# Optimization experiments

Hardware: AMD Instinct MI355X
Metric: run time of the kernel (lower is better)

Reference implementation:

```python
import jax, jax.numpy as jnp
import numpy as np

EPS = 1e-6


def ln_fwd(x, gamma, beta):
    # layernorm over last dim (biased variance), per TTT ln_fwd
    mu = x.mean(-1, keepdims=True)
    var = x.var(-1, keepdims=True)
    xh = (x - mu) * jax.lax.rsqrt(var + EPS)
    return gamma * xh + beta


def ln_fused_l2_bwd(x, l2_target, gamma, beta):
    # grad of 0.5*||LN(x) - target||^2 w.r.t. x, fused (per TTT ln_fused_l2_bwd)
    D = x.shape[-1]
    mu = x.mean(-1, keepdims=True)
    var = x.var(-1, keepdims=True)
    std = jnp.sqrt(var + EPS)
    xh = (x - mu) / std
    y = gamma * xh + beta
    gxh = (y - l2_target) * gamma
    z = (D * gxh - gxh.sum(-1, keepdims=True) - xh * (gxh * xh).sum(-1, keepdims=True)) / (D * std)
    return z


def setup_inputs() -> dict:
    key = jax.random.key(0)
    ks = jax.random.split(key, 5)
    B, nh, nmb, mbs, hd = 8, 8, 256, 16, 64
    XQ = jax.random.normal(ks[0], (B, nh, nmb, mbs, hd), jnp.float32)
    XK = jax.random.normal(ks[1], (B, nh, nmb, mbs, hd), jnp.float32)
    XV = jax.random.normal(ks[2], (B, nh, nmb, mbs, hd), jnp.float32)
    # eta = small positive per-token learning rates (ttt_base_lr/head_dim scale)
    eta = jax.random.uniform(ks[3], (B, nh, nmb, mbs, mbs), jnp.float32) * (1.0 / hd)
    W1 = jax.random.normal(ks[4], (nh, hd, hd), jnp.float32) * 0.02
    b1 = jnp.zeros((nh, 1, hd), jnp.float32)
    ln_weight = jnp.ones((nh * hd,), jnp.float32)
    ln_bias = jnp.zeros((nh * hd,), jnp.float32)
    return {"XQ": XQ, "XK": XK, "XV": XV, "eta": eta, "W1": W1, "b1": b1,
            "ln_weight": ln_weight, "ln_bias": ln_bias}


def reference(XQ, XK, XV, eta, W1, b1, ln_weight, ln_bias):
    B, nh, nmb, mbs, hd = XQ.shape
    lnw = ln_weight.reshape(nh, 1, hd)
    lnb = ln_bias.reshape(nh, 1, hd)
    W1_0 = jnp.broadcast_to(W1[None], (B, nh, hd, hd))
    b1_0 = jnp.broadcast_to(b1[None], (B, nh, 1, hd))
    tril = jnp.tril(jnp.ones((mbs, mbs), XQ.dtype))

    def step(carry, inp):
        W1s, b1s = carry               # [B,nh,hd,hd], [B,nh,1,hd]
        xq, xk, xv, et = inp           # [B,nh,mbs,hd] x3, [B,nh,mbs,mbs]
        Z1 = xk @ W1s + b1s
        g = ln_fused_l2_bwd(Z1, xv - xk, lnw, lnb)          # grad_l_wrt_Z1
        Attn1 = tril * (xq @ jnp.swapaxes(xk, -1, -2))      # causal QK^T
        b1_bar = b1s - (tril * et) @ g
        Z1_bar = xq @ W1s - (et * Attn1) @ g + b1_bar
        last_eta = et[..., -1, :, None]                     # [B,nh,mbs,1]
        W1_last = W1s - jnp.swapaxes(last_eta * xk, -1, -2) @ g
        b1_last = b1s - jnp.sum(last_eta * g, axis=-2, keepdims=True)
        out = xq + ln_fwd(Z1_bar, lnw, lnb)
        return (W1_last, b1_last), out

    xs = (jnp.moveaxis(XQ, 2, 0), jnp.moveaxis(XK, 2, 0),
          jnp.moveaxis(XV, 2, 0), jnp.moveaxis(eta, 2, 0))
    _, outs = jax.lax.scan(step, (W1_0, b1_0), xs)
    # outs: [nmb,B,nh,mbs,hd] -> [B,nmb,mbs,nh,hd] -> [B,L,width]
    return jnp.transpose(outs, (1, 0, 3, 2, 4)).reshape(B, nmb * mbs, nh * hd)
```

## Files before the change

kernel.cpp:

```cpp
#include <hip/hip_runtime.h>
#include <hip/hip_bf16.h>

typedef __attribute__((ext_vector_type(8))) short short8;
typedef __attribute__((ext_vector_type(4))) short short4_t;
typedef __attribute__((ext_vector_type(4))) float f32x4;

constexpr int MBS = 16, HD = 64, NMB = 256;

#define MFMA32(a, b, c) __builtin_amdgcn_mfma_f32_16x16x32_bf16(a, b, c, 0, 0, 0)
#define TR_READ(dst, addr, IMM) \
    asm volatile("ds_read_b64_tr_b16 %0, %1 offset:" IMM : "=&v"(dst) : "v"(addr) : "memory")

union U4S8 { unsigned u[4]; short8 s; };
union U2S4 { unsigned u[2]; short4_t s; };
union FI { float f; int i; };

__device__ inline unsigned pkbf(float a, float b) {
    union { __hip_bfloat162 h; unsigned u; } c;
    c.h = __float22bfloat162_rn(make_float2(a, b));
    return c.u;
}
__device__ inline short8 cmb(short4_t a, short4_t b) {
    short8 r;
    r[0]=a[0]; r[1]=a[1]; r[2]=a[2]; r[3]=a[3];
    r[4]=b[0]; r[5]=b[1]; r[6]=b[2]; r[7]=b[3];
    return r;
}
__device__ inline float dpp16(float x) {
    FI v; v.f = x; FI t;
    t.i = __builtin_amdgcn_update_dpp(0, v.i, 0xB1, 0xf, 0xf, true);  v.f += t.f;
    t.i = __builtin_amdgcn_update_dpp(0, v.i, 0x4E, 0xf, 0xf, true);  v.f += t.f;
    t.i = __builtin_amdgcn_update_dpp(0, v.i, 0x124, 0xf, 0xf, true); v.f += t.f;
    t.i = __builtin_amdgcn_update_dpp(0, v.i, 0x128, 0xf, 0xf, true); v.f += t.f;
    return v.f;
}
__device__ inline void bar() {
    __builtin_amdgcn_sched_barrier(0);
    asm volatile("s_waitcnt lgkmcnt(0)" ::: "memory");
    __builtin_amdgcn_s_barrier();
    __builtin_amdgcn_sched_barrier(0);
}

__global__ __launch_bounds__(256) void ttt_scan(
    const float* __restrict__ gXQ, const float* __restrict__ gXK,
    const float* __restrict__ gXV, const float* __restrict__ gETA,
    const float* __restrict__ gW1, const float* __restrict__ gB1,
    const float* __restrict__ gLNW, const float* __restrict__ gLNB,
    float* __restrict__ gOUT)
{
    __shared__ __align__(16) short sWt[64 * 72];
    __shared__ __align__(16) short bxk[16 * 72];
    __shared__ __align__(16) short bxq[16 * 72];
    __shared__ __align__(16) short sGt[2048];
    __shared__ __align__(16) short sXKe[2048];
    __shared__ __align__(16) short sE[16 * 40];
    __shared__ __align__(16) float sZ1[16 * 68];
    __shared__ __align__(16) float sZb[16 * 68];
    __shared__ __align__(16) float sAttn[16 * 20];
    __shared__ __align__(16) float sEta[2][256];

    const int t  = threadIdx.x;
    const int s  = t >> 4;
    const int dt = t & 15;
    const int lane = t & 63;
    const int w  = t >> 6;
    const int gq = lane >> 4;
    const int lc = lane & 15;
    const int bh = blockIdx.x, b = bh >> 3, h = bh & 7;

    const float* xqg = gXQ + (size_t)bh * (NMB * MBS * HD);
    const float* xkg = gXK + (size_t)bh * (NMB * MBS * HD);
    const float* xvg = gXV + (size_t)bh * (NMB * MBS * HD);
    const float* etg = gETA + (size_t)bh * (NMB * MBS * MBS);

    for (int i = t; i < 2048; i += 256) { sGt[i] = 0; sXKe[i] = 0; }
    for (int i = t; i < 16 * 40; i += 256) sE[i] = 0;

    f32x4 Wacc[4];
#pragma unroll
    for (int ct = 0; ct < 4; ++ct) {
#pragma unroll
        for (int r = 0; r < 4; ++r)
            Wacc[ct][r] = gW1[h * 4096 + (16 * w + 4 * gq + r) * 64 + 16 * ct + lc];
        U2S4 wp;
        wp.u[0] = pkbf(Wacc[ct][0], Wacc[ct][1]);
        wp.u[1] = pkbf(Wacc[ct][2], Wacc[ct][3]);
        *(short4_t*)&sWt[(16 * ct + lc) * 72 + 16 * w + 4 * gq] = wp.s;
    }
    float b1v = gB1[h * 64 + 16 * w + lc];

    const float4 gam = *(const float4*)&gLNW[h * 64 + dt * 4];
    const float4 bet = *(const float4*)&gLNB[h * 64 + dt * 4];
    const float ga[4] = {gam.x, gam.y, gam.z, gam.w};
    const float ba[4] = {bet.x, bet.y, bet.z, bet.w};
    float c1a[4], gba[4];
    float sc1 = 0.f;
#pragma unroll
    for (int c = 0; c < 4; ++c) {
        c1a[c] = ga[c] * ga[c];
        gba[c] = ga[c] * ba[c];
        sc1 += c1a[c];
    }
    sc1 = dpp16(sc1);

    const int ecol = (gq < 2) ? 8 * gq : 0;

    float4 pq = *(const float4*)&xqg[t * 4];
    float4 pk = *(const float4*)&xkg[t * 4];
    float4 pv = *(const float4*)&xvg[t * 4];
    float4 pe = make_float4(0.f, 0.f, 0.f, 0.f);
    if (t < 64) pe = *(const float4*)&etg[t * 4];

    { U2S4 u_; u_.u[0]=pkbf(pk.x,pk.y); u_.u[1]=pkbf(pk.z,pk.w);
      *(short4_t*)&bxk[s * 72 + dt * 4] = u_.s; }
    { U2S4 u_; u_.u[0]=pkbf(pq.x,pq.y); u_.u[1]=pkbf(pq.z,pq.w);
      *(short4_t*)&bxq[s * 72 + dt * 4] = u_.s; }
    if (t < 64) *(float4*)&sEta[0][t * 4] = pe;
    float t2c[4];
    {
        const float pva[4] = {pv.x, pv.y, pv.z, pv.w};
        const float pka_[4] = {pk.x, pk.y, pk.z, pk.w};
#pragma unroll
        for (int c = 0; c < 4; ++c)
            t2c[c] = fmaf(-ga[c], pva[c] - pka_[c], gba[c]);
    }
    float4 pkc = pk;
    float4 pq_out = pq;
    float4 pq_prev_out;

    __syncthreads();

#pragma unroll 1
    for (int m = 0; m < NMB; ++m) {
        const int p = m & 1;

        if (m + 1 < NMB) {
            const size_t o = (size_t)(m + 1) * (MBS * HD) + t * 4;
            pq = *(const float4*)&xqg[o];
            pk = *(const float4*)&xkg[o];
            pv = *(const float4*)&xvg[o];
            if (t < 64) pe = *(const float4*)&etg[(size_t)(m + 1) * (MBS * MBS) + t * 4];
        }

        f32x4 z1a; z1a[0]=b1v; z1a[1]=b1v; z1a[2]=b1v; z1a[3]=b1v;
        f32x4 zqa = z1a;
        const short8 ak0 = *(const short8*)&bxk[lc * 72 + gq * 8];
        const short8 ak1 = *(const short8*)&bxk[lc * 72 + gq * 8 + 32];
        const short8 aq0 = *(const short8*)&bxq[lc * 72 + gq * 8];
        const short8 aq1 = *(const short8*)&bxq[lc * 72 + gq * 8 + 32];
        const short8 bw0 = *(const short8*)&sWt[(16 * w + lc) * 72 + gq * 8];
        const short8 bw1 = *(const short8*)&sWt[(16 * w + lc) * 72 + gq * 8 + 32];
        z1a = MFMA32(ak0, bw0, z1a); z1a = MFMA32(ak1, bw1, z1a);
        zqa = MFMA32(aq0, bw0, zqa); zqa = MFMA32(aq1, bw1, zqa);
#pragma unroll
        for (int r = 0; r < 4; ++r) sZ1[(4 * gq + r) * 68 + 16 * w + lc] = z1a[r];
        if (w == 3) {
            f32x4 zz; zz[0]=0.f; zz[1]=0.f; zz[2]=0.f; zz[3]=0.f;
            zz = MFMA32(aq0, ak0, zz); zz = MFMA32(aq1, ak1, zz);
#pragma unroll
            for (int r = 0; r < 4; ++r) sAttn[(4 * gq + r) * 20 + lc] = zz[r];
        }

        if (m > 0) {
            f32x4 zbr = *(f32x4*)&sZb[s * 68 + dt * 4];
            float T1 = 0.f, T2 = 0.f;
#pragma unroll
            for (int c = 0; c < 4; ++c) { T1 += zbr[c]; T2 = fmaf(zbr[c], zbr[c], T2); }
            T1 = dpp16(T1); T2 = dpp16(T2);
            const float mu2   = T1 * (1.f / 64.f);
            const float rstd2 = rsqrtf(T2 * (1.f / 64.f) - mu2 * mu2 + 1e-6f);
            const float pqa[4] = {pq_prev_out.x, pq_prev_out.y, pq_prev_out.z, pq_prev_out.w};
            float o[4];
#pragma unroll
            for (int c = 0; c < 4; ++c)
                o[c] = pqa[c] + fmaf(ga[c], (zbr[c] - mu2) * rstd2, ba[c]);
            const size_t oi = ((size_t)b * 4096 + (size_t)(m - 1) * 16 + s) * 512 + h * 64 + dt * 4;
            *(float4*)&gOUT[oi] = make_float4(o[0], o[1], o[2], o[3]);
        }
        bar();

        f32x4 z = *(f32x4*)&sZ1[s * 68 + dt * 4];
        float S1=0.f,S2=0.f,S3=0.f,S4=0.f,S5=0.f,S6=0.f;
#pragma unroll
        for (int c = 0; c < 4; ++c) {
            const float zc = z[c], c1z = c1a[c] * zc, t2 = t2c[c];
            S1 += zc;  S2 = fmaf(zc, zc, S2);
            S3 += c1z; S4 = fmaf(c1z, zc, S4);
            S5 += t2;  S6 = fmaf(t2, zc, S6);
        }
        S1 = dpp16(S1); S2 = dpp16(S2); S3 = dpp16(S3);
        S4 = dpp16(S4); S5 = dpp16(S5); S6 = dpp16(S6);
        const float mu   = S1 * (1.f / 64.f);
        const float rstd = rsqrtf(S2 * (1.f / 64.f) - mu * mu + 1e-6f);
        const float r1 = rstd * (S3 - mu * sc1) + S5;
        const float r2 = rstd * rstd * (S4 - 2.f * mu * S3 + mu * mu * sc1)
                       + rstd * (S6 - mu * S5);
        const float cf = rstd * (1.f / 64.f);
        float g[4];
#pragma unroll
        for (int c = 0; c < 4; ++c) {
            const float xh = (z[c] - mu) * rstd;
            const float gx = fmaf(c1a[c], xh, t2c[c]);
            g[c] = (fmaf(64.f, gx, -r1) - xh * r2) * cf;
        }

        const float le = sEta[p][240 + s];
        const int tb = (s >> 2) * 256 + (dt >> 2) * 64 + (s & 3) * 16 + (dt & 3) * 4;
        { U2S4 gp; gp.u[0]=pkbf(g[0],g[1]); gp.u[1]=pkbf(g[2],g[3]);
          *(short4_t*)&sGt[tb] = gp.s; }
        { U2S4 kp; kp.u[0]=pkbf(-le*pkc.x,-le*pkc.y); kp.u[1]=pkbf(-le*pkc.z,-le*pkc.w);
          *(short4_t*)&sXKe[tb] = kp.s; }

        if (dt < 4) {
            f32x4 at = *(f32x4*)&sAttn[s * 20 + dt * 4];
            f32x4 ev = *(f32x4*)&sEta[p][s * 16 + dt * 4];
            U2S4 ep;
            float x[4];
#pragma unroll
            for (int c = 0; c < 4; ++c) {
                const int cc = 4 * dt + c;
                x[c] = (cc <= s) ? -ev[c] * (1.f + at[c]) : 0.f;
            }
            ep.u[0] = pkbf(x[0], x[1]); ep.u[1] = pkbf(x[2], x[3]);
            *(short4_t*)&sE[s * 40 + 4 * dt] = ep.s;
        }
        bar();

        const unsigned gbase = (unsigned)(size_t)&sGt[0] + 1024u * gq + 8u * lc;
        const unsigned ebase = gbase + 128u * (unsigned)w;
        const unsigned kbase = (unsigned)(size_t)&sXKe[0] + 1024u * gq + 8u * lc
                             + 128u * (unsigned)w;
        short4_t elo, ehi, al, ah;
        short4_t bl0, bh0, bl1, bh1, bl2, bh2, bl3, bh3;
        TR_READ(elo, ebase, "0");   TR_READ(ehi, ebase, "512");
        TR_READ(al,  kbase, "0");   TR_READ(ah,  kbase, "512");
        TR_READ(bl0, gbase, "0");   TR_READ(bh0, gbase, "512");
        TR_READ(bl1, gbase, "128"); TR_READ(bh1, gbase, "640");
        TR_READ(bl2, gbase, "256"); TR_READ(bh2, gbase, "768");
        TR_READ(bl3, gbase, "384"); TR_READ(bh3, gbase, "896");
        const short8 aE = *(const short8*)&sE[lc * 40 + gq * 8];
        const f32x4 le0 = *(const f32x4*)&sEta[p][240 + ecol];
        const f32x4 le1 = *(const f32x4*)&sEta[p][244 + ecol];
        U4S8 aL;
        {
            const float lv[8] = {le0[0], le0[1], le0[2], le0[3], le1[0], le1[1], le1[2], le1[3]};
#pragma unroll
            for (int pp = 0; pp < 4; ++pp) {
                const float y0 = (gq < 2) ? -lv[2 * pp] : 0.f;
                const float y1 = (gq < 2) ? -lv[2 * pp + 1] : 0.f;
                aL.u[pp] = pkbf(y0, y1);
            }
        }
        asm volatile("s_waitcnt lgkmcnt(0)" ::: "memory");
        __builtin_amdgcn_sched_barrier(0);

        const short8 bgw = cmb(elo, ehi);
        f32x4 zb = MFMA32(aE, bgw, zqa);
#pragma unroll
        for (int r = 0; r < 4; ++r) sZb[(4 * gq + r) * 68 + 16 * w + lc] = zb[r];

        const short8 aK = cmb(al, ah);
        Wacc[0] = MFMA32(aK, cmb(bl0, bh0), Wacc[0]);
        Wacc[1] = MFMA32(aK, cmb(bl1, bh1), Wacc[1]);
        Wacc[2] = MFMA32(aK, cmb(bl2, bh2), Wacc[2]);
        Wacc[3] = MFMA32(aK, cmb(bl3, bh3), Wacc[3]);
        {
            f32x4 d0; d0[0]=0.f; d0[1]=0.f; d0[2]=0.f; d0[3]=0.f;
            d0 = MFMA32(aL.s, bgw, d0);
            b1v += d0[0];
        }
#pragma unroll
        for (int ct = 0; ct < 4; ++ct) {
            U2S4 wp;
            wp.u[0] = pkbf(Wacc[ct][0], Wacc[ct][1]);
            wp.u[1] = pkbf(Wacc[ct][2], Wacc[ct][3]);
            *(short4_t*)&sWt[(16 * ct + lc) * 72 + 16 * w + 4 * gq] = wp.s;
        }

        if (m + 1 < NMB) {
            { U2S4 u_; u_.u[0]=pkbf(pk.x,pk.y); u_.u[1]=pkbf(pk.z,pk.w);
              *(short4_t*)&bxk[s * 72 + dt * 4] = u_.s; }
            { U2S4 u_; u_.u[0]=pkbf(pq.x,pq.y); u_.u[1]=pkbf(pq.z,pq.w);
              *(short4_t*)&bxq[s * 72 + dt * 4] = u_.s; }
            if (t < 64) *(float4*)&sEta[p ^ 1][t * 4] = pe;
#pragma unroll
            for (int c = 0; c < 4; ++c) {
                const float pva[4] = {pv.x, pv.y, pv.z, pv.w};
                const float pka_[4] = {pk.x, pk.y, pk.z, pk.w};
                t2c[c] = fmaf(-ga[c], pva[c] - pka_[c], gba[c]);
            }
            pkc = pk;
        }
        pq_prev_out = pq_out;
        pq_out = pq;
        bar();
    }

    {
        f32x4 zbr = *(f32x4*)&sZb[s * 68 + dt * 4];
        float T1 = 0.f, T2 = 0.f;
#pragma unroll
        for (int c = 0; c < 4; ++c) { T1 += zbr[c]; T2 = fmaf(zbr[c], zbr[c], T2); }
        T1 = dpp16(T1); T2 = dpp16(T2);
        const float mu2   = T1 * (1.f / 64.f);
        const float rstd2 = rsqrtf(T2 * (1.f / 64.f) - mu2 * mu2 + 1e-6f);
        const float pqa[4] = {pq_prev_out.x, pq_prev_out.y, pq_prev_out.z, pq_prev_out.w};
        float o[4];
#pragma unroll
        for (int c = 0; c < 4; ++c)
            o[c] = pqa[c] + fmaf(ga[c], (zbr[c] - mu2) * rstd2, ba[c]);
        const size_t oi = ((size_t)b * 4096 + (size_t)(NMB - 1) * 16 + s) * 512 + h * 64 + dt * 4;
        *(float4*)&gOUT[oi] = make_float4(o[0], o[1], o[2], o[3]);
    }
}

extern "C" void kernel_launch(void* const* d_in, const int* in_sizes, int n_in,
                              void* d_out, int out_size, void* d_ws, size_t ws_size,
                              hipStream_t stream) {
    const float* XQ  = (const float*)d_in[0];
    const float* XK  = (const float*)d_in[1];
    const float* XV  = (const float*)d_in[2];
    const float* ETA = (const float*)d_in[3];
    const float* W1  = (const float*)d_in[4];
    const float* B1  = (const float*)d_in[5];
    const float* LNW = (const float*)d_in[6];
    const float* LNB = (const float*)d_in[7];
    float* OUT = (float*)d_out;

    const int n_chains = in_sizes[0] / (NMB * MBS * HD);
    ttt_scan<<<n_chains, 256, 0, stream>>>(XQ, XK, XV, ETA, W1, B1, LNW, LNB, OUT);
}
```

Before: 380.2 us.

## Pack two scan chains per 512-thread block with a shared zero buffer

Each workgroup now runs two independent (batch, head) recurrences, 256 threads each, with per-chain shared-memory structs, and launches half as many blocks. The zero-padded halves of the gradient and key transposed buffers are replaced by one shared zero region that the upper lane groups read from, shrinking per-chain LDS. Block-wide barriers now synchronize both chains together, which couples their progress and may add stall time. The likely aim is to pack chains into fewer workgroups on a grid of only 64 blocks.

```diff
diff --git a/kernel.cpp b/kernel.cpp
--- a/kernel.cpp
+++ b/kernel.cpp
@@ -41,40 +41,49 @@
     __builtin_amdgcn_sched_barrier(0);
 }
 
-__global__ __launch_bounds__(256) void ttt_scan(
+struct __align__(16) ChainSM {
+    short sWt[64 * 72];
+    short bxk[16 * 72];
+    short bxq[16 * 72];
+    short sGt[1024];
+    short sXKe[1024];
+    short sE[16 * 40];
+    float sZ1[16 * 68];
+    float sZb[16 * 68];
+    float sAttn[16 * 20];
+    float sEta[2][256];
+};
+
+__global__ __launch_bounds__(512) void ttt_scan(
     const float* __restrict__ gXQ, const float* __restrict__ gXK,
     const float* __restrict__ gXV, const float* __restrict__ gETA,
     const float* __restrict__ gW1, const float* __restrict__ gB1,
     const float* __restrict__ gLNW, const float* __restrict__ gLNB,
     float* __restrict__ gOUT)
 {
-    __shared__ __align__(16) short sWt[64 * 72];
-    __shared__ __align__(16) short bxk[16 * 72];
-    __shared__ __align__(16) short bxq[16 * 72];
-    __shared__ __align__(16) short sGt[2048];
-    __shared__ __align__(16) short sXKe[2048];
-    __shared__ __align__(16) short sE[16 * 40];
-    __shared__ __align__(16) float sZ1[16 * 68];
-    __shared__ __align__(16) float sZb[16 * 68];
-    __shared__ __align__(16) float sAttn[16 * 20];
-    __shared__ __align__(16) float sEta[2][256];
-
-    const int t  = threadIdx.x;
+    __shared__ ChainSM ch[2];
+    __shared__ __align__(16) short sZERO[1024];
+
+    const int gt = threadIdx.x;
+    const int cw = gt >> 8;
+    const int t  = gt & 255;
+    ChainSM& C = ch[cw];
+
     const int s  = t >> 4;
     const int dt = t & 15;
     const int lane = t & 63;
-    const int w  = t >> 6;
+    const int w  = (t >> 6) & 3;
     const int gq = lane >> 4;
     const int lc = lane & 15;
-    const int bh = blockIdx.x, b = bh >> 3, h = bh & 7;
+    const int bh = blockIdx.x * 2 + cw, b = bh >> 3, h = bh & 7;
 
     const float* xqg = gXQ + (size_t)bh * (NMB * MBS * HD);
     const float* xkg = gXK + (size_t)bh * (NMB * MBS * HD);
     const float* xvg = gXV + (size_t)bh * (NMB * MBS * HD);
     const float* etg = gETA + (size_t)bh * (NMB * MBS * MBS);
 
-    for (int i = t; i < 2048; i += 256) { sGt[i] = 0; sXKe[i] = 0; }
-    for (int i = t; i < 16 * 40; i += 256) sE[i] = 0;
+    for (int i = gt; i < 1024; i += 512) sZERO[i] = 0;
+    for (int i = t; i < 16 * 40; i += 256) C.sE[i] = 0;
 
     f32x4 Wacc[4];
 #pragma unroll
@@ -85,7 +94,7 @@
         U2S4 wp;
         wp.u[0] = pkbf(Wacc[ct][0], Wacc[ct][1]);
         wp.u[1] = pkbf(Wacc[ct][2], Wacc[ct][3]);
-        *(short4_t*)&sWt[(16 * ct + lc) * 72 + 16 * w + 4 * gq] = wp.s;
+        *(short4_t*)&C.sWt[(16 * ct + lc) * 72 + 16 * w + 4 * gq] = wp.s;
     }
     float b1v = gB1[h * 64 + 16 * w + lc];
 
@@ -112,10 +121,10 @@
     if (t < 64) pe = *(const float4*)&etg[t * 4];
 
     { U2S4 u_; u_.u[0]=pkbf(pk.x,pk.y); u_.u[1]=pkbf(pk.z,pk.w);
-      *(short4_t*)&bxk[s * 72 + dt * 4] = u_.s; }
+      *(short4_t*)&C.bxk[s * 72 + dt * 4] = u_.s; }
     { U2S4 u_; u_.u[0]=pkbf(pq.x,pq.y); u_.u[1]=pkbf(pq.z,pq.w);
-      *(short4_t*)&bxq[s * 72 + dt * 4] = u_.s; }
-    if (t < 64) *(float4*)&sEta[0][t * 4] = pe;
+      *(short4_t*)&C.bxq[s * 72 + dt * 4] = u_.s; }
+    if (t < 64) *(float4*)&C.sEta[0][t * 4] = pe;
     float t2c[4];
     {
         const float pva[4] = {pv.x, pv.y, pv.z, pv.w};
@@ -144,25 +153,25 @@
 
         f32x4 z1a; z1a[0]=b1v; z1a[1]=b1v; z1a[2]=b1v; z1a[3]=b1v;
         f32x4 zqa = z1a;
-        const short8 ak0 = *(const short8*)&bxk[lc * 72 + gq * 8];
-        const short8 ak1 = *(const short8*)&bxk[lc * 72 + gq * 8 + 32];
-        const short8 aq0 = *(const short8*)&bxq[lc * 72 + gq * 8];
-        const short8 aq1 = *(const short8*)&bxq[lc * 72 + gq * 8 + 32];
-        const short8 bw0 = *(const short8*)&sWt[(16 * w + lc) * 72 + gq * 8];
-        const short8 bw1 = *(const short8*)&sWt[(16 * w + lc) * 72 + gq * 8 + 32];
+        const short8 ak0 = *(const short8*)&C.bxk[lc * 72 + gq * 8];
+        const short8 ak1 = *(const short8*)&C.bxk[lc * 72 + gq * 8 + 32];
+        const short8 aq0 = *(const short8*)&C.bxq[lc * 72 + gq * 8];
+        const short8 aq1 = *(const short8*)&C.bxq[lc * 72 + gq * 8 + 32];
+        const short8 bw0 = *(const short8*)&C.sWt[(16 * w + lc) * 72 + gq * 8];
+        const short8 bw1 = *(const short8*)&C.sWt[(16 * w + lc) * 72 + gq * 8 + 32];
         z1a = MFMA32(ak0, bw0, z1a); z1a = MFMA32(ak1, bw1, z1a);
         zqa = MFMA32(aq0, bw0, zqa); zqa = MFMA32(aq1, bw1, zqa);
 #pragma unroll
-        for (int r = 0; r < 4; ++r) sZ1[(4 * gq + r) * 68 + 16 * w + lc] = z1a[r];
+        for (int r = 0; r < 4; ++r) C.sZ1[(4 * gq + r) * 68 + 16 * w + lc] = z1a[r];
         if (w == 3) {
             f32x4 zz; zz[0]=0.f; zz[1]=0.f; zz[2]=0.f; zz[3]=0.f;
             zz = MFMA32(aq0, ak0, zz); zz = MFMA32(aq1, ak1, zz);
 #pragma unroll
-            for (int r = 0; r < 4; ++r) sAttn[(4 * gq + r) * 20 + lc] = zz[r];
+            for (int r = 0; r < 4; ++r) C.sAttn[(4 * gq + r) * 20 + lc] = zz[r];
         }
 
         if (m > 0) {
-            f32x4 zbr = *(f32x4*)&sZb[s * 68 + dt * 4];
+            f32x4 zbr = *(f32x4*)&C.sZb[s * 68 + dt * 4];
             float T1 = 0.f, T2 = 0.f;
 #pragma unroll
             for (int c = 0; c < 4; ++c) { T1 += zbr[c]; T2 = fmaf(zbr[c], zbr[c], T2); }
@@ -179,7 +188,7 @@
         }
         bar();
 
-        f32x4 z = *(f32x4*)&sZ1[s * 68 + dt * 4];
+        f32x4 z = *(f32x4*)&C.sZ1[s * 68 + dt * 4];
         float S1=0.f,S2=0.f,S3=0.f,S4=0.f,S5=0.f,S6=0.f;
 #pragma unroll
         for (int c = 0; c < 4; ++c) {
@@ -204,16 +213,16 @@
             g[c] = (fmaf(64.f, gx, -r1) - xh * r2) * cf;
         }
 
-        const float le = sEta[p][240 + s];
+        const float le = C.sEta[p][240 + s];
         const int tb = (s >> 2) * 256 + (dt >> 2) * 64 + (s & 3) * 16 + (dt & 3) * 4;
         { U2S4 gp; gp.u[0]=pkbf(g[0],g[1]); gp.u[1]=pkbf(g[2],g[3]);
-          *(short4_t*)&sGt[tb] = gp.s; }
+          *(short4_t*)&C.sGt[tb] = gp.s; }
         { U2S4 kp; kp.u[0]=pkbf(-le*pkc.x,-le*pkc.y); kp.u[1]=pkbf(-le*pkc.z,-le*pkc.w);
-          *(short4_t*)&sXKe[tb] = kp.s; }
+          *(short4_t*)&C.sXKe[tb] = kp.s; }
 
         if (dt < 4) {
-            f32x4 at = *(f32x4*)&sAttn[s * 20 + dt * 4];
-            f32x4 ev = *(f32x4*)&sEta[p][s * 16 + dt * 4];
+            f32x4 at = *(f32x4*)&C.sAttn[s * 20 + dt * 4];
+            f32x4 ev = *(f32x4*)&C.sEta[p][s * 16 + dt * 4];
             U2S4 ep;
             float x[4];
 #pragma unroll
@@ -222,14 +231,18 @@
                 x[c] = (cc <= s) ? -ev[c] * (1.f + at[c]) : 0.f;
             }
             ep.u[0] = pkbf(x[0], x[1]); ep.u[1] = pkbf(x[2], x[3]);
-            *(short4_t*)&sE[s * 40 + 4 * dt] = ep.s;
+            *(short4_t*)&C.sE[s * 40 + 4 * dt] = ep.s;
         }
         bar();
 
-        const unsigned gbase = (unsigned)(size_t)&sGt[0] + 1024u * gq + 8u * lc;
+        const unsigned gbase = (gq < 2)
+            ? ((unsigned)(size_t)&C.sGt[0] + 1024u * gq + 8u * lc)
+            : ((unsigned)(size_t)&sZERO[0] + 8u * lc);
         const unsigned ebase = gbase + 128u * (unsigned)w;
-        const unsigned kbase = (unsigned)(size_t)&sXKe[0] + 1024u * gq + 8u * lc
-                             + 128u * (unsigned)w;
+        const unsigned kbase = ((gq < 2)
+            ? ((unsigned)(size_t)&C.sXKe[0] + 1024u * gq)
+            : ((unsigned)(size_t)&sZERO[0]))
+            + 8u * lc + 128u * (unsigned)w;
         short4_t elo, ehi, al, ah;
         short4_t bl0, bh0, bl1, bh1, bl2, bh2, bl3, bh3;
         TR_READ(elo, ebase, "0");   TR_READ(ehi, ebase, "512");
@@ -238,9 +251,9 @@
         TR_READ(bl1, gbase, "128"); TR_READ(bh1, gbase, "640");
         TR_READ(bl2, gbase, "256"); TR_READ(bh2, gbase, "768");
         TR_READ(bl3, gbase, "384"); TR_READ(bh3, gbase, "896");
-        const short8 aE = *(const short8*)&sE[lc * 40 + gq * 8];
-        const f32x4 le0 = *(const f32x4*)&sEta[p][240 + ecol];
-        const f32x4 le1 = *(const f32x4*)&sEta[p][244 + ecol];
+        const short8 aE = *(const short8*)&C.sE[lc * 40 + gq * 8];
+        const f32x4 le0 = *(const f32x4*)&C.sEta[p][240 + ecol];
+        const f32x4 le1 = *(const f32x4*)&C.sEta[p][244 + ecol];
         U4S8 aL;
         {
             const float lv[8] = {le0[0], le0[1], le0[2], le0[3], le1[0], le1[1], le1[2], le1[3]};
@@ -257,7 +270,7 @@
         const short8 bgw = cmb(elo, ehi);
         f32x4 zb = MFMA32(aE, bgw, zqa);
 #pragma unroll
-        for (int r = 0; r < 4; ++r) sZb[(4 * gq + r) * 68 + 16 * w + lc] = zb[r];
+        for (int r = 0; r < 4; ++r) C.sZb[(4 * gq + r) * 68 + 16 * w + lc] = zb[r];
 
         const short8 aK = cmb(al, ah);
         Wacc[0] = MFMA32(aK, cmb(bl0, bh0), Wacc[0]);
@@ -274,15 +287,15 @@
             U2S4 wp;
             wp.u[0] = pkbf(Wacc[ct][0], Wacc[ct][1]);
             wp.u[1] = pkbf(Wacc[ct][2], Wacc[ct][3]);
-            *(short4_t*)&sWt[(16 * ct + lc) * 72 + 16 * w + 4 * gq] = wp.s;
+            *(short4_t*)&C.sWt[(16 * ct + lc) * 72 + 16 * w + 4 * gq] = wp.s;
         }
 
         if (m + 1 < NMB) {
             { U2S4 u_; u_.u[0]=pkbf(pk.x,pk.y); u_.u[1]=pkbf(pk.z,pk.w);
-              *(short4_t*)&bxk[s * 72 + dt * 4] = u_.s; }
+              *(short4_t*)&C.bxk[s * 72 + dt * 4] = u_.s; }
             { U2S4 u_; u_.u[0]=pkbf(pq.x,pq.y); u_.u[1]=pkbf(pq.z,pq.w);
-              *(short4_t*)&bxq[s * 72 + dt * 4] = u_.s; }
-            if (t < 64) *(float4*)&sEta[p ^ 1][t * 4] = pe;
+              *(short4_t*)&C.bxq[s * 72 + dt * 4] = u_.s; }
+            if (t < 64) *(float4*)&C.sEta[p ^ 1][t * 4] = pe;
 #pragma unroll
             for (int c = 0; c < 4; ++c) {
                 const float pva[4] = {pv.x, pv.y, pv.z, pv.w};
@@ -297,7 +310,7 @@
     }
 
     {
-        f32x4 zbr = *(f32x4*)&sZb[s * 68 + dt * 4];
+        f32x4 zbr = *(f32x4*)&C.sZb[s * 68 + dt * 4];
         float T1 = 0.f, T2 = 0.f;
 #pragma unroll
         for (int c = 0; c < 4; ++c) { T1 += zbr[c]; T2 = fmaf(zbr[c], zbr[c], T2); }
@@ -328,5 +341,5 @@
     float* OUT = (float*)d_out;
 
     const int n_chains = in_sizes[0] / (NMB * MBS * HD);
-    ttt_scan<<<n_chains, 256, 0, stream>>>(XQ, XK, XV, ETA, W1, B1, LNW, LNB, OUT);
-}
+    ttt_scan<<<n_chains / 2, 512, 0, stream>>>(XQ, XK, XV, ETA, W1, B1, LNW, LNB, OUT);
+}
```

Result: slower. 489.6 us (+28.8%).

## Use 16x16x16 MFMA for K=16 products and fuse eta-attention mask build

Applied to the files above, without the earlier changes.

The reductions over the 16-token minibatch were padded to K=32 for the 16x16x32 bf16 MFMA, using zero-filled halves of the shared buffers. They now use the native 16x16x16 bf16 MFMA, which halves the gradient and key transpose-read traffic and the shared buffer sizes, and removes the zero-initialisation. The masked eta*(1+Attn) matrix is now built directly from the QK^T MFMA result by wave 3, which drops the sAttn round trip and the separate pass by other threads. The risk is that the inline-asm fallback for the MFMA carries s_nop padding, and all of wave 3's extra work sits before the barrier.

```diff
diff --git a/kernel.cpp b/kernel.cpp
--- a/kernel.cpp
+++ b/kernel.cpp
@@ -8,10 +8,21 @@
 constexpr int MBS = 16, HD = 64, NMB = 256;
 
 #define MFMA32(a, b, c) __builtin_amdgcn_mfma_f32_16x16x32_bf16(a, b, c, 0, 0, 0)
+
+#if __has_builtin(__builtin_amdgcn_mfma_f32_16x16x16bf16_1k)
+#define MFMA16(a, b, c) __builtin_amdgcn_mfma_f32_16x16x16bf16_1k(a, b, c, 0, 0, 0)
+#else
+__device__ inline f32x4 mfma16_asm(short4_t a, short4_t b, f32x4 c) {
+    asm volatile("v_mfma_f32_16x16x16_bf16 %0, %1, %2, %0\n\ts_nop 7\n\ts_nop 7"
+                 : "+v"(c) : "v"(a), "v"(b));
+    return c;
+}
+#define MFMA16(a, b, c) mfma16_asm(a, b, c)
+#endif
+
 #define TR_READ(dst, addr, IMM) \
     asm volatile("ds_read_b64_tr_b16 %0, %1 offset:" IMM : "=&v"(dst) : "v"(addr) : "memory")
 
-union U4S8 { unsigned u[4]; short8 s; };
 union U2S4 { unsigned u[2]; short4_t s; };
 union FI { float f; int i; };
 
@@ -20,12 +31,7 @@
     c.h = __float22bfloat162_rn(make_float2(a, b));
     return c.u;
 }
-__device__ inline short8 cmb(short4_t a, short4_t b) {
-    short8 r;
-    r[0]=a[0]; r[1]=a[1]; r[2]=a[2]; r[3]=a[3];
-    r[4]=b[0]; r[5]=b[1]; r[6]=b[2]; r[7]=b[3];
-    return r;
-}
+__device__ inline short bf16s(float x) { return (short)(pkbf(x, 0.f) & 0xffffu); }
 __device__ inline float dpp16(float x) {
     FI v; v.f = x; FI t;
     t.i = __builtin_amdgcn_update_dpp(0, v.i, 0xB1, 0xf, 0xf, true);  v.f += t.f;
@@ -51,12 +57,11 @@
     __shared__ __align__(16) short sWt[64 * 72];
     __shared__ __align__(16) short bxk[16 * 72];
     __shared__ __align__(16) short bxq[16 * 72];
-    __shared__ __align__(16) short sGt[2048];
-    __shared__ __align__(16) short sXKe[2048];
-    __shared__ __align__(16) short sE[16 * 40];
+    __shared__ __align__(16) short sGt[1024];
+    __shared__ __align__(16) short sXKe[1024];
+    __shared__ __align__(16) short sE[16 * 20];
     __shared__ __align__(16) float sZ1[16 * 68];
     __shared__ __align__(16) float sZb[16 * 68];
-    __shared__ __align__(16) float sAttn[16 * 20];
     __shared__ __align__(16) float sEta[2][256];
 
     const int t  = threadIdx.x;
@@ -73,9 +78,6 @@
     const float* xvg = gXV + (size_t)bh * (NMB * MBS * HD);
     const float* etg = gETA + (size_t)bh * (NMB * MBS * MBS);
 
-    for (int i = t; i < 2048; i += 256) { sGt[i] = 0; sXKe[i] = 0; }
-    for (int i = t; i < 16 * 40; i += 256) sE[i] = 0;
-
     f32x4 Wacc[4];
 #pragma unroll
     for (int ct = 0; ct < 4; ++ct) {
@@ -102,8 +104,6 @@
         sc1 += c1a[c];
     }
     sc1 = dpp16(sc1);
-
-    const int ecol = (gq < 2) ? 8 * gq : 0;
 
     float4 pq = *(const float4*)&xqg[t * 4];
     float4 pk = *(const float4*)&xkg[t * 4];
@@ -154,11 +154,17 @@
         zqa = MFMA32(aq0, bw0, zqa); zqa = MFMA32(aq1, bw1, zqa);
 #pragma unroll
         for (int r = 0; r < 4; ++r) sZ1[(4 * gq + r) * 68 + 16 * w + lc] = z1a[r];
+
         if (w == 3) {
             f32x4 zz; zz[0]=0.f; zz[1]=0.f; zz[2]=0.f; zz[3]=0.f;
             zz = MFMA32(aq0, ak0, zz); zz = MFMA32(aq1, ak1, zz);
 #pragma unroll
-            for (int r = 0; r < 4; ++r) sAttn[(4 * gq + r) * 20 + lc] = zz[r];
+            for (int r = 0; r < 4; ++r) {
+                const int row = 4 * gq + r;
+                const float ev = sEta[p][row * 16 + lc];
+                const float x = (lc <= row) ? -ev * (1.f + zz[r]) : 0.f;
+                sE[row * 20 + lc] = bf16s(x);
+            }
         }
 
         if (m > 0) {
@@ -210,63 +216,40 @@
           *(short4_t*)&sGt[tb] = gp.s; }
         { U2S4 kp; kp.u[0]=pkbf(-le*pkc.x,-le*pkc.y); kp.u[1]=pkbf(-le*pkc.z,-le*pkc.w);
           *(short4_t*)&sXKe[tb] = kp.s; }
-
-        if (dt < 4) {
-            f32x4 at = *(f32x4*)&sAttn[s * 20 + dt * 4];
-            f32x4 ev = *(f32x4*)&sEta[p][s * 16 + dt * 4];
-            U2S4 ep;
-            float x[4];
-#pragma unroll
-            for (int c = 0; c < 4; ++c) {
-                const int cc = 4 * dt + c;
-                x[c] = (cc <= s) ? -ev[c] * (1.f + at[c]) : 0.f;
-            }
-            ep.u[0] = pkbf(x[0], x[1]); ep.u[1] = pkbf(x[2], x[3]);
-            *(short4_t*)&sE[s * 40 + 4 * dt] = ep.s;
-        }
         bar();
 
-        const unsigned gbase = (unsigned)(size_t)&sGt[0] + 1024u * gq + 8u * lc;
-        const unsigned ebase = gbase + 128u * (unsigned)w;
-        const unsigned kbase = (unsigned)(size_t)&sXKe[0] + 1024u * gq + 8u * lc
-                             + 128u * (unsigned)w;
-        short4_t elo, ehi, al, ah;
-        short4_t bl0, bh0, bl1, bh1, bl2, bh2, bl3, bh3;
-        TR_READ(elo, ebase, "0");   TR_READ(ehi, ebase, "512");
-        TR_READ(al,  kbase, "0");   TR_READ(ah,  kbase, "512");
-        TR_READ(bl0, gbase, "0");   TR_READ(bh0, gbase, "512");
-        TR_READ(bl1, gbase, "128"); TR_READ(bh1, gbase, "640");
-        TR_READ(bl2, gbase, "256"); TR_READ(bh2, gbase, "768");
-        TR_READ(bl3, gbase, "384"); TR_READ(bh3, gbase, "896");
-        const short8 aE = *(const short8*)&sE[lc * 40 + gq * 8];
-        const f32x4 le0 = *(const f32x4*)&sEta[p][240 + ecol];
-        const f32x4 le1 = *(const f32x4*)&sEta[p][244 + ecol];
-        U4S8 aL;
-        {
-            const float lv[8] = {le0[0], le0[1], le0[2], le0[3], le1[0], le1[1], le1[2], le1[3]};
-#pragma unroll
-            for (int pp = 0; pp < 4; ++pp) {
-                const float y0 = (gq < 2) ? -lv[2 * pp] : 0.f;
-                const float y1 = (gq < 2) ? -lv[2 * pp + 1] : 0.f;
-                aL.u[pp] = pkbf(y0, y1);
-            }
-        }
+        const unsigned gbase = (unsigned)(size_t)&sGt[0] + 512u * gq + 8u * lc;
+        const unsigned kbase = (unsigned)(size_t)&sXKe[0] + 512u * gq + 128u * (unsigned)w + 8u * lc;
+        short4_t bg0, bg1, bg2, bg3, aK;
+        TR_READ(bg0, gbase, "0");
+        TR_READ(bg1, gbase, "128");
+        TR_READ(bg2, gbase, "256");
+        TR_READ(bg3, gbase, "384");
+        TR_READ(aK,  kbase, "0");
+        const short4_t aE = *(const short4_t*)&sE[lc * 20 + gq * 4];
+        const f32x4 lv = *(const f32x4*)&sEta[p][240 + 4 * gq];
+        U2S4 aL;
+        aL.u[0] = pkbf(-lv[0], -lv[1]);
+        aL.u[1] = pkbf(-lv[2], -lv[3]);
         asm volatile("s_waitcnt lgkmcnt(0)" ::: "memory");
         __builtin_amdgcn_sched_barrier(0);
 
-        const short8 bgw = cmb(elo, ehi);
-        f32x4 zb = MFMA32(aE, bgw, zqa);
+        short4_t bgw = bg0;
+        if (w == 1) bgw = bg1;
+        else if (w == 2) bgw = bg2;
+        else if (w == 3) bgw = bg3;
+
+        f32x4 zb = MFMA16(aE, bgw, zqa);
 #pragma unroll
         for (int r = 0; r < 4; ++r) sZb[(4 * gq + r) * 68 + 16 * w + lc] = zb[r];
 
-        const short8 aK = cmb(al, ah);
-        Wacc[0] = MFMA32(aK, cmb(bl0, bh0), Wacc[0]);
-        Wacc[1] = MFMA32(aK, cmb(bl1, bh1), Wacc[1]);
-        Wacc[2] = MFMA32(aK, cmb(bl2, bh2), Wacc[2]);
-        Wacc[3] = MFMA32(aK, cmb(bl3, bh3), Wacc[3]);
+        Wacc[0] = MFMA16(aK, bg0, Wacc[0]);
+        Wacc[1] = MFMA16(aK, bg1, Wacc[1]);
+        Wacc[2] = MFMA16(aK, bg2, Wacc[2]);
+        Wacc[3] = MFMA16(aK, bg3, Wacc[3]);
         {
             f32x4 d0; d0[0]=0.f; d0[1]=0.f; d0[2]=0.f; d0[3]=0.f;
-            d0 = MFMA32(aL.s, bgw, d0);
+            d0 = MFMA16(aL.s, bgw, d0);
             b1v += d0[0];
         }
 #pragma unroll
```

Result: no change. 374.7 us (-1.4%).
